# Optimization experiments

Hardware: AMD Instinct MI355X
Metric: run time of the kernel (lower is better)

The kernel has to match this reference:

```python
import jax, jax.numpy as jnp
import numpy as np

NUM_GROUPS = 32
EPS = 1e-5
NUM_HEAD = 8
DIM_HEAD = 64


def group_norm(t, w, b):
    # t: (B, N, C) tokens; GroupNorm over (N, C//G) within each group
    B, N, C = t.shape
    g = t.reshape(B, N, NUM_GROUPS, C // NUM_GROUPS)
    mu = g.mean(axis=(1, 3), keepdims=True)
    var = g.var(axis=(1, 3), keepdims=True)
    g = (g - mu) * jax.lax.rsqrt(var + EPS)
    return g.reshape(B, N, C) * w + b


def setup_inputs() -> dict:
    key = jax.random.key(0)
    ks = jax.random.split(key, 4)
    B, C, H, W = 2, 512, 48, 48
    hidden = NUM_HEAD * DIM_HEAD
    return {
        "x": jax.random.normal(ks[0], (B, C, H, W), dtype=jnp.float32),
        "gn1_w": jnp.ones((C,), jnp.float32),
        "gn1_b": jnp.zeros((C,), jnp.float32),
        "w_qkv": jax.random.normal(ks[1], (3 * hidden, C), jnp.float32) * 0.02,
        "mem_kv": jax.random.normal(ks[2], (2, NUM_HEAD, DIM_HEAD, 4), jnp.float32),
        "w_out": jax.random.normal(ks[3], (C, hidden), jnp.float32) * 0.02,
        "b_out": jnp.zeros((C,), jnp.float32),
        "gn2_w": jnp.ones((C,), jnp.float32),
        "gn2_b": jnp.zeros((C,), jnp.float32),
    }


def reference(x, gn1_w, gn1_b, w_qkv, mem_kv, w_out, b_out, gn2_w, gn2_b):
    B, C, H, W = x.shape
    N = H * W
    hidden = NUM_HEAD * DIM_HEAD
    scale = DIM_HEAD ** -0.5

    # tokens: (B, N, C)
    t = x.reshape(B, C, N).transpose(0, 2, 1)
    t = group_norm(t, gn1_w, gn1_b)

    # 1x1 conv QKV projection == per-token GEMM
    qkv = t @ w_qkv.T  # (B, N, 3*hidden)
    q, k, v = jnp.split(qkv, 3, axis=-1)

    def to_heads(a):  # (B, N, hidden) -> (B, nh, N, dh)
        return a.reshape(B, N, NUM_HEAD, DIM_HEAD).transpose(0, 2, 1, 3)

    q, k, v = to_heads(q), to_heads(k), to_heads(v)

    # memory kv prepended along sequence axis: (nh, dh, nkv) -> (1, nh, nkv, dh)
    mk = jnp.broadcast_to(mem_kv[0].transpose(0, 2, 1)[None], (B, NUM_HEAD, mem_kv.shape[-1], DIM_HEAD))
    mv = jnp.broadcast_to(mem_kv[1].transpose(0, 2, 1)[None], (B, NUM_HEAD, mem_kv.shape[-1], DIM_HEAD))
    k = jnp.concatenate([mk, k], axis=2)
    v = jnp.concatenate([mv, v], axis=2)

    scores = jnp.einsum('bhid,bhjd->bhij', q, k) * scale  # (B, nh, N, N+nkv)
    attn = jax.nn.softmax(scores, axis=-1)  # dropout = identity in eval
    o = jnp.einsum('bhij,bhjd->bhid', attn, v)  # (B, nh, N, dh)

    o = o.transpose(0, 2, 1, 3).reshape(B, N, hidden)
    o = o @ w_out.T + b_out  # 1x1 out conv
    o = group_norm(o, gn2_w, gn2_b)
    return o.transpose(0, 2, 1).reshape(B, C, H, W)
```

## Files before the change

### kernel.cpp

```cpp
#include <hip/hip_runtime.h>
#include <hip/hip_bf16.h>

typedef short short8 __attribute__((ext_vector_type(8)));
typedef float f32x4 __attribute__((ext_vector_type(4)));

#define GPTR(x) ((const __attribute__((address_space(1))) void*)(x))
#define LPTR(x) ((__attribute__((address_space(3))) void*)(x))

static __device__ __forceinline__ unsigned short f2bf(float f) {
  __hip_bfloat16 h = __float2bfloat16(f);
  return __builtin_bit_cast(unsigned short, h);
}
static __device__ __forceinline__ float bf2f(unsigned short u) {
  unsigned int v = ((unsigned int)u) << 16;
  return __builtin_bit_cast(float, v);
}

static __device__ __forceinline__ void block_reduce2(float& s, float& q) {
#pragma unroll
  for (int o = 32; o > 0; o >>= 1) { s += __shfl_down(s, o); q += __shfl_down(q, o); }
  __shared__ float rs[4], rq[4];
  int tid = threadIdx.x;
  if ((tid & 63) == 0) { rs[tid >> 6] = s; rq[tid >> 6] = q; }
  __syncthreads();
  if (tid == 0) {
    s = rs[0] + rs[1] + rs[2] + rs[3];
    q = rq[0] + rq[1] + rq[2] + rq[3];
  }
}

__global__ __launch_bounds__(256) void prep_gn1_kernel(
    const float* __restrict__ wqkv, const float* __restrict__ wout,
    const float* __restrict__ memkv, const float* __restrict__ x,
    unsigned short* __restrict__ wq, unsigned short* __restrict__ wo,
    unsigned short* __restrict__ Kb, unsigned short* __restrict__ Vb,
    float2* __restrict__ part1) {
  int blk = blockIdx.x;
  if (blk < 4128) {
    int i = blk * 256 + threadIdx.x;
    if (i < 786432) {
      wq[i] = f2bf(wqkv[i]);
    } else if (i < 1048576) {
      int j = i - 786432;
      wo[j] = f2bf(wout[j]);
    } else if (i < 1056768) {
      int t = i - 1048576;
      int d = t & 63, j = (t >> 6) & 3, h = (t >> 8) & 7, b = (t >> 11) & 1, s = t >> 12;
      unsigned short bv = f2bf(memkv[((s * 8 + h) * 64 + d) * 4 + j]);
      unsigned short* dst = (s == 0) ? Kb : Vb;
      dst[((size_t)(b * 8 + h) * 2308 + j) * 64 + d] = bv;
    }
  } else {
    int bgc = blk - 4128;
    const float4* base = (const float4*)x + (size_t)bgc * 1152;
    float s = 0.f, q = 0.f;
    for (int i = threadIdx.x; i < 1152; i += 256) {
      float4 v = base[i];
      s += v.x + v.y + v.z + v.w;
      q += v.x * v.x + v.y * v.y + v.z * v.z + v.w * v.w;
    }
    block_reduce2(s, q);
    if (threadIdx.x == 0) part1[bgc] = make_float2(s, q);
  }
}

__global__ __launch_bounds__(256) void tnorm_kernel(const float* __restrict__ x,
    const float* __restrict__ gw, const float* __restrict__ gb,
    const float2* __restrict__ part1, unsigned short* __restrict__ t) {
  __shared__ float tile[32][33];
  int n0 = blockIdx.x * 32, c0 = blockIdx.y * 32, b = blockIdx.z;
  int g0 = c0 >> 4;
  float mu2[2], rs2[2];
#pragma unroll
  for (int gg = 0; gg < 2; gg++) {
    float s = 0.f, q = 0.f;
    const float2* p = part1 + (size_t)(b * 32 + g0 + gg) * 8;
#pragma unroll
    for (int k = 0; k < 8; k++) { float2 v = p[k]; s += v.x; q += v.y; }
    float mu = s / 36864.f;
    float var = q / 36864.f - mu * mu;
    mu2[gg] = mu;
    rs2[gg] = rsqrtf(var + 1e-5f);
  }
  int tx = threadIdx.x & 31, ty = threadIdx.x >> 5;
#pragma unroll
  for (int r = 0; r < 4; r++) {
    int c = c0 + ty + r * 8;
    tile[ty + r * 8][tx] = x[((size_t)(b * 512 + c)) * 2304 + n0 + tx];
  }
  __syncthreads();
  int gg = tx >> 4;
#pragma unroll
  for (int r = 0; r < 4; r++) {
    int n = n0 + ty + r * 8;
    int c = c0 + tx;
    float v = tile[tx][ty + r * 8];
    t[((size_t)(b * 2304 + n)) * 512 + c] = f2bf((v - mu2[gg]) * rs2[gg] * gw[c] + gb[c]);
  }
}

__global__ __launch_bounds__(256) void gemm_qkv_kernel(
    const unsigned short* __restrict__ A, const unsigned short* __restrict__ Bw,
    unsigned short* __restrict__ Qb, unsigned short* __restrict__ Kb,
    unsigned short* __restrict__ Vb) {
  __shared__ __attribute__((aligned(16))) unsigned short As[128 * 32];
  __shared__ __attribute__((aligned(16))) unsigned short Bs[128 * 32];
  int m0 = blockIdx.x * 128, o0 = blockIdx.y * 128;
  int tid = threadIdx.x, lane = tid & 63, wave = tid >> 6;
  int quad = lane >> 4, l15 = lane & 15;
  int wm = wave & 1, wn = wave >> 1;
  f32x4 acc[4][4] = {};
  for (int k0 = 0; k0 < 512; k0 += 32) {
    __syncthreads();
#pragma unroll
    for (int c = 0; c < 2; c++) {
      int q = tid + c * 256;
      int row = q >> 2, cc = q & 3;
      __builtin_amdgcn_global_load_lds(GPTR(A + (size_t)(m0 + row) * 512 + k0 + cc * 8),
                                       LPTR(As + q * 8), 16, 0, 0);
      __builtin_amdgcn_global_load_lds(GPTR(Bw + (size_t)(o0 + row) * 512 + k0 + cc * 8),
                                       LPTR(Bs + q * 8), 16, 0, 0);
    }
    __syncthreads();
    short8 af[4], bf[4];
#pragma unroll
    for (int i = 0; i < 4; i++) af[i] = *(const short8*)(As + (wm * 64 + i * 16 + l15) * 32 + quad * 8);
#pragma unroll
    for (int j = 0; j < 4; j++) bf[j] = *(const short8*)(Bs + (wn * 64 + j * 16 + l15) * 32 + quad * 8);
#pragma unroll
    for (int i = 0; i < 4; i++)
#pragma unroll
      for (int j = 0; j < 4; j++)
        acc[i][j] = __builtin_amdgcn_mfma_f32_16x16x32_bf16(af[i], bf[j], acc[i][j], 0, 0, 0);
  }
#pragma unroll
  for (int i = 0; i < 4; i++) {
#pragma unroll
    for (int j = 0; j < 4; j++) {
      int colo = o0 + wn * 64 + j * 16 + l15;
      int part = colo >> 9, rr = colo & 511, h = rr >> 6, d = rr & 63;
#pragma unroll
      for (int reg = 0; reg < 4; reg++) {
        int m = m0 + wm * 64 + i * 16 + quad * 4 + reg;
        int b = (m >= 2304) ? 1 : 0;
        int n = m - b * 2304;
        unsigned short bv = f2bf(acc[i][j][reg]);
        if (part == 0)      Qb[((size_t)(b * 8 + h) * 2304 + n) * 64 + d] = bv;
        else if (part == 1) Kb[((size_t)(b * 8 + h) * 2308 + 4 + n) * 64 + d] = bv;
        else                Vb[((size_t)(b * 8 + h) * 2308 + 4 + n) * 64 + d] = bv;
      }
    }
  }
}

__global__ __launch_bounds__(256) void vt_kernel(const unsigned short* __restrict__ Vb,
                                                 unsigned short* __restrict__ Vt) {
  __shared__ unsigned short tile[64 * 68];
  int ct = blockIdx.x, bh = blockIdx.y;
  int tid = threadIdx.x;
#pragma unroll
  for (int c = 0; c < 2; c++) {
    int q = tid + c * 256;
    int row = q >> 3, c8 = q & 7;
    int gk = ct * 64 + row;
    uint4 v = make_uint4(0, 0, 0, 0);
    if (gk < 2308) v = *(const uint4*)(Vb + ((size_t)bh * 2308 + gk) * 64 + c8 * 8);
    *(uint2*)(tile + row * 68 + c8 * 8)     = make_uint2(v.x, v.y);
    *(uint2*)(tile + row * 68 + c8 * 8 + 4) = make_uint2(v.z, v.w);
  }
  __syncthreads();
#pragma unroll
  for (int c = 0; c < 2; c++) {
    int q = tid + c * 256;
    int d = q >> 3, c8 = q & 7;
    unsigned short tmp[8];
#pragma unroll
    for (int jj = 0; jj < 8; jj++) tmp[jj] = tile[(c8 * 8 + jj) * 68 + d];
    *(uint4*)(Vt + ((size_t)bh * 64 + d) * 2368 + ct * 64 + c8 * 8) = *(uint4*)tmp;
  }
}

__global__ __launch_bounds__(256) void attn_kernel(
    const unsigned short* __restrict__ Qb, const unsigned short* __restrict__ Kb,
    const unsigned short* __restrict__ Vt,
    unsigned short* __restrict__ Opart, float* __restrict__ Lbuf) {
  __shared__ __attribute__((aligned(16))) unsigned short Ks[64 * 72];
  __shared__ __attribute__((aligned(16))) unsigned short Vts[64 * 72];
  __shared__ __attribute__((aligned(16))) unsigned short Ps[128 * 72];
  int qt = blockIdx.x, bh = blockIdx.y, sp = blockIdx.z;
  int m0 = qt * 128;
  int kt0 = sp * 10, kt1 = (kt0 + 10 < 37) ? kt0 + 10 : 37;
  const unsigned short* Qh = Qb + (size_t)bh * 2304 * 64;
  const unsigned short* Kh = Kb + (size_t)bh * 2308 * 64;
  const unsigned short* VtH = Vt + (size_t)bh * 64 * 2368;
  int tid = threadIdx.x, lane = tid & 63, wave = tid >> 6;
  int quad = lane >> 4, l15 = lane & 15;
  const float CS = 0.18033688011112042f;

  short8 qf[2][2];
#pragma unroll
  for (int i = 0; i < 2; i++)
#pragma unroll
    for (int s = 0; s < 2; s++)
      qf[i][s] = *(const short8*)(Qh + (size_t)(m0 + wave * 32 + i * 16 + l15) * 64 + s * 32 + quad * 8);

  f32x4 oacc[2][4] = {};
  float lsum[2][4] = {};

  for (int kt = kt0; kt < kt1; kt++) {
    __syncthreads();
#pragma unroll
    for (int c = 0; c < 2; c++) {
      int q = tid + c * 256;
      int krow = q >> 3, c8 = q & 7;
      int gk = kt * 64 + krow;
      uint4 kv = make_uint4(0, 0, 0, 0);
      if (gk < 2308) kv = *(const uint4*)(Kh + (size_t)gk * 64 + c8 * 8);
      *(uint4*)(Ks + krow * 72 + c8 * 8) = kv;
      uint4 vv = *(const uint4*)(VtH + (size_t)krow * 2368 + kt * 64 + c8 * 8);
      *(uint4*)(Vts + krow * 72 + c8 * 8) = vv;
    }
    __syncthreads();
    f32x4 sacc[2][4] = {};
#pragma unroll
    for (int s = 0; s < 2; s++) {
      short8 kf[4];
#pragma unroll
      for (int j = 0; j < 4; j++) kf[j] = *(const short8*)(Ks + (j * 16 + l15) * 72 + s * 32 + quad * 8);
#pragma unroll
      for (int i = 0; i < 2; i++)
#pragma unroll
        for (int j = 0; j < 4; j++)
          sacc[i][j] = __builtin_amdgcn_mfma_f32_16x16x32_bf16(qf[i][s], kf[j], sacc[i][j], 0, 0, 0);
    }
    if (kt == 36) {
#pragma unroll
      for (int j = 0; j < 4; j++) {
        bool ok = (kt * 64 + j * 16 + l15) < 2308;
        if (!ok) {
#pragma unroll
          for (int i = 0; i < 2; i++)
#pragma unroll
            for (int r = 0; r < 4; r++) sacc[i][j][r] = -1e30f;
        }
      }
    }
#pragma unroll
    for (int i = 0; i < 2; i++) {
#pragma unroll
      for (int r = 0; r < 4; r++) {
        int prow = (wave * 32 + i * 16 + quad * 4 + r) * 72;
#pragma unroll
        for (int j = 0; j < 4; j++) {
          float p = exp2f(sacc[i][j][r] * CS);
          lsum[i][r] += p;
          Ps[prow + j * 16 + l15] = f2bf(p);
        }
      }
    }
#pragma unroll
    for (int s = 0; s < 2; s++) {
      short8 ap[2];
#pragma unroll
      for (int i = 0; i < 2; i++)
        ap[i] = *(const short8*)(Ps + (wave * 32 + i * 16 + l15) * 72 + s * 32 + quad * 8);
#pragma unroll
      for (int jo = 0; jo < 4; jo++) {
        short8 bv = *(const short8*)(Vts + (jo * 16 + l15) * 72 + s * 32 + quad * 8);
#pragma unroll
        for (int i = 0; i < 2; i++)
          oacc[i][jo] = __builtin_amdgcn_mfma_f32_16x16x32_bf16(ap[i], bv, oacc[i][jo], 0, 0, 0);
      }
    }
  }
#pragma unroll
  for (int i = 0; i < 2; i++)
#pragma unroll
    for (int r = 0; r < 4; r++) {
      float v = lsum[i][r];
#pragma unroll
      for (int o = 1; o < 16; o <<= 1) v += __shfl_xor(v, o);
      lsum[i][r] = v;
    }
  size_t obase = (size_t)(sp * 16 + bh) * 2304;
#pragma unroll
  for (int i = 0; i < 2; i++) {
#pragma unroll
    for (int r = 0; r < 4; r++) {
      int row = m0 + wave * 32 + i * 16 + quad * 4 + r;
#pragma unroll
      for (int jo = 0; jo < 4; jo++)
        Opart[(obase + row) * 64 + jo * 16 + l15] = f2bf(oacc[i][jo][r]);
      if (l15 == 0) Lbuf[obase + row] = lsum[i][r];
    }
  }
}

__global__ __launch_bounds__(256) void combine_kernel(
    const unsigned short* __restrict__ Opart, const float* __restrict__ Lbuf,
    unsigned short* __restrict__ Ot) {
  int rg = blockIdx.x * 4 + (threadIdx.x >> 6);
  int d = threadIdx.x & 63;
  int bh = rg / 2304, row = rg - bh * 2304;
  int b = bh >> 3, h = bh & 7;
  float num = 0.f, den = 0.f;
#pragma unroll
  for (int s = 0; s < 4; s++) {
    size_t ri = ((size_t)(s * 16 + bh) * 2304 + row);
    den += Lbuf[ri];
    num += bf2f(Opart[ri * 64 + d]);
  }
  Ot[((size_t)(b * 2304 + row)) * 512 + h * 64 + d] = f2bf(num / den);
}

__global__ __launch_bounds__(256) void gemm_out_kernel(
    const unsigned short* __restrict__ A, const unsigned short* __restrict__ Bw,
    const float* __restrict__ bias, float* __restrict__ y,
    float* __restrict__ p2s, float* __restrict__ p2q) {
  __shared__ __attribute__((aligned(16))) unsigned short As[128 * 32];
  __shared__ __attribute__((aligned(16))) unsigned short Bs[128 * 32];
  __shared__ float sgrp[8], qgrp[8];
  int m0 = blockIdx.x * 128, o0 = blockIdx.y * 128;
  int tid = threadIdx.x, lane = tid & 63, wave = tid >> 6;
  int quad = lane >> 4, l15 = lane & 15;
  int wm = wave & 1, wn = wave >> 1;
  if (tid < 8) { sgrp[tid] = 0.f; qgrp[tid] = 0.f; }
  f32x4 acc[4][4] = {};
  for (int k0 = 0; k0 < 512; k0 += 32) {
    __syncthreads();
#pragma unroll
    for (int c = 0; c < 2; c++) {
      int q = tid + c * 256;
      int row = q >> 2, cc = q & 3;
      __builtin_amdgcn_global_load_lds(GPTR(A + (size_t)(m0 + row) * 512 + k0 + cc * 8),
                                       LPTR(As + q * 8), 16, 0, 0);
      __builtin_amdgcn_global_load_lds(GPTR(Bw + (size_t)(o0 + row) * 512 + k0 + cc * 8),
                                       LPTR(Bs + q * 8), 16, 0, 0);
    }
    __syncthreads();
    short8 af[4], bf[4];
#pragma unroll
    for (int i = 0; i < 4; i++) af[i] = *(const short8*)(As + (wm * 64 + i * 16 + l15) * 32 + quad * 8);
#pragma unroll
    for (int j = 0; j < 4; j++) bf[j] = *(const short8*)(Bs + (wn * 64 + j * 16 + l15) * 32 + quad * 8);
#pragma unroll
    for (int i = 0; i < 4; i++)
#pragma unroll
      for (int j = 0; j < 4; j++)
        acc[i][j] = __builtin_amdgcn_mfma_f32_16x16x32_bf16(af[i], bf[j], acc[i][j], 0, 0, 0);
  }
  float ss[4] = {}, qq[4] = {};
#pragma unroll
  for (int i = 0; i < 4; i++) {
#pragma unroll
    for (int j = 0; j < 4; j++) {
      int colo = o0 + wn * 64 + j * 16 + l15;
      float bb = bias[colo];
#pragma unroll
      for (int reg = 0; reg < 4; reg++) {
        int m = m0 + wm * 64 + i * 16 + quad * 4 + reg;
        float v = acc[i][j][reg] + bb;
        y[(size_t)m * 512 + colo] = v;
        ss[j] += v;
        qq[j] += v * v;
      }
    }
  }
#pragma unroll
  for (int j = 0; j < 4; j++) {
#pragma unroll
    for (int o = 1; o < 64; o <<= 1) { ss[j] += __shfl_xor(ss[j], o); qq[j] += __shfl_xor(qq[j], o); }
  }
  if (lane == 0) {
#pragma unroll
    for (int j = 0; j < 4; j++) {
      atomicAdd(&sgrp[wn * 4 + j], ss[j]);
      atomicAdd(&qgrp[wn * 4 + j], qq[j]);
    }
  }
  __syncthreads();
  if (tid < 8) {
    int b = (m0 >= 2304) ? 1 : 0;
    int g = b * 32 + (o0 >> 4) + tid;
    atomicAdd(&p2s[g], sgrp[tid]);
    atomicAdd(&p2q[g], qgrp[tid]);
  }
}

__global__ __launch_bounds__(256) void gn2_final_kernel(const float* __restrict__ y,
    const float* __restrict__ gw, const float* __restrict__ gb,
    const float* __restrict__ p2s, const float* __restrict__ p2q,
    float* __restrict__ out) {
  __shared__ float tile[32][33];
  int n0 = blockIdx.x * 32, c0 = blockIdx.y * 32, b = blockIdx.z;
  int g0 = c0 >> 4;
  float mu2[2], rs2[2];
#pragma unroll
  for (int gg = 0; gg < 2; gg++) {
    float s = p2s[b * 32 + g0 + gg], q = p2q[b * 32 + g0 + gg];
    float mu = s / 36864.f;
    float var = q / 36864.f - mu * mu;
    mu2[gg] = mu;
    rs2[gg] = rsqrtf(var + 1e-5f);
  }
  int tx = threadIdx.x & 31, ty = threadIdx.x >> 5;
#pragma unroll
  for (int r = 0; r < 4; r++) {
    int n = n0 + ty + r * 8;
    tile[ty + r * 8][tx] = y[((size_t)(b * 2304 + n)) * 512 + c0 + tx];
  }
  __syncthreads();
#pragma unroll
  for (int r = 0; r < 4; r++) {
    int c = c0 + ty + r * 8;
    int gg = (ty + r * 8) >> 4;
    float v = tile[tx][ty + r * 8];
    out[((size_t)(b * 512 + c)) * 2304 + n0 + tx] = (v - mu2[gg]) * rs2[gg] * gw[c] + gb[c];
  }
}

extern "C" void kernel_launch(void* const* d_in, const int* in_sizes, int n_in,
                              void* d_out, int out_size, void* d_ws, size_t ws_size,
                              hipStream_t stream) {
  const float* x     = (const float*)d_in[0];
  const float* gn1w  = (const float*)d_in[1];
  const float* gn1b  = (const float*)d_in[2];
  const float* wqkv  = (const float*)d_in[3];
  const float* memkv = (const float*)d_in[4];
  const float* wout  = (const float*)d_in[5];
  const float* bout  = (const float*)d_in[6];
  const float* gn2w  = (const float*)d_in[7];
  const float* gn2b  = (const float*)d_in[8];
  float* out = (float*)d_out;

  char* ws = (char*)d_ws;
  float2* part1        = (float2*)(ws + 0);
  float* p2s           = (float*)(ws + 4096);
  float* p2q           = (float*)(ws + 4352);
  unsigned short* wqB  = (unsigned short*)(ws + 69632);
  unsigned short* woB  = (unsigned short*)(ws + 1642496);
  unsigned short* tB   = (unsigned short*)(ws + 2166784);
  unsigned short* Qb   = (unsigned short*)(ws + 6885376);
  unsigned short* Kb   = (unsigned short*)(ws + 11603968);
  unsigned short* Vb   = (unsigned short*)(ws + 16330752);
  unsigned short* Ot   = (unsigned short*)(ws + 21057536);
  float* y             = (float*)(ws + 25776128);
  unsigned short* Vt   = (unsigned short*)(ws + 35213312);
  unsigned short* Opart= (unsigned short*)(ws + 40062976);
  float* Lbuf          = (float*)(ws + 58937344);

  prep_gn1_kernel<<<4640, 256, 0, stream>>>(wqkv, wout, memkv, x, wqB, woB, Kb, Vb, part1);
  tnorm_kernel<<<dim3(72, 16, 2), 256, 0, stream>>>(x, gn1w, gn1b, part1, tB);
  gemm_qkv_kernel<<<dim3(36, 12), 256, 0, stream>>>(tB, wqB, Qb, Kb, Vb);
  vt_kernel<<<dim3(37, 16), 256, 0, stream>>>(Vb, Vt);
  attn_kernel<<<dim3(18, 16, 4), 256, 0, stream>>>(Qb, Kb, Vt, Opart, Lbuf);
  combine_kernel<<<9216, 256, 0, stream>>>(Opart, Lbuf, Ot);
  hipMemsetAsync(ws + 4096, 0, 512, stream);
  gemm_out_kernel<<<dim3(36, 4), 256, 0, stream>>>(Ot, woB, bout, y, p2s, p2q);
  gn2_final_kernel<<<dim3(72, 16, 2), 256, 0, stream>>>(y, gn2w, gn2b, p2s, p2q, out);
}
```

Measured before the change: 193.8 us.

## Write V transposed from QKV GEMM, fuse prep into tnorm, vectorize combine

The QKV GEMM epilogue now writes V straight into the transposed Vt layout, and the separate vt transpose kernel and the Vb buffer are removed. The weight conversion and memory-kv setup are merged into the tnorm kernel launch, and the GN1 statistics move to their own small kernel. The combine kernel now handles four channels per thread with vector loads and stores. Together these cut one launch and one round trip of V through memory. The risk is that the Vt padding columns past the real key length are no longer zeroed explicitly, and the GEMM epilogue's transposed stores are strided.

```diff
diff --git a/kernel.cpp b/kernel.cpp
--- a/kernel.cpp
+++ b/kernel.cpp
@@ -29,80 +29,80 @@
   }
 }
 
-__global__ __launch_bounds__(256) void prep_gn1_kernel(
+__global__ __launch_bounds__(256) void gn1_stats_kernel(const float* __restrict__ x,
+                                                        float2* __restrict__ part1) {
+  int bgc = blockIdx.x;
+  const float4* base = (const float4*)x + (size_t)bgc * 1152;
+  float s = 0.f, q = 0.f;
+  for (int i = threadIdx.x; i < 1152; i += 256) {
+    float4 v = base[i];
+    s += v.x + v.y + v.z + v.w;
+    q += v.x * v.x + v.y * v.y + v.z * v.z + v.w * v.w;
+  }
+  block_reduce2(s, q);
+  if (threadIdx.x == 0) part1[bgc] = make_float2(s, q);
+}
+
+__global__ __launch_bounds__(256) void tnorm_prep_kernel(const float* __restrict__ x,
+    const float* __restrict__ gw, const float* __restrict__ gb,
+    const float2* __restrict__ part1, unsigned short* __restrict__ t,
     const float* __restrict__ wqkv, const float* __restrict__ wout,
-    const float* __restrict__ memkv, const float* __restrict__ x,
+    const float* __restrict__ memkv,
     unsigned short* __restrict__ wq, unsigned short* __restrict__ wo,
-    unsigned short* __restrict__ Kb, unsigned short* __restrict__ Vb,
-    float2* __restrict__ part1) {
+    unsigned short* __restrict__ Kb, unsigned short* __restrict__ Vt) {
+  __shared__ float tile[32][33];
   int blk = blockIdx.x;
-  if (blk < 4128) {
-    int i = blk * 256 + threadIdx.x;
+  if (blk < 2304) {
+    int n0 = (blk % 72) * 32, c0 = ((blk / 72) & 15) * 32, b = blk / 1152;
+    int g0 = c0 >> 4;
+    float mu2[2], rs2[2];
+#pragma unroll
+    for (int gg = 0; gg < 2; gg++) {
+      float s = 0.f, q = 0.f;
+      const float2* p = part1 + (size_t)(b * 32 + g0 + gg) * 8;
+#pragma unroll
+      for (int k = 0; k < 8; k++) { float2 v = p[k]; s += v.x; q += v.y; }
+      float mu = s / 36864.f;
+      float var = q / 36864.f - mu * mu;
+      mu2[gg] = mu;
+      rs2[gg] = rsqrtf(var + 1e-5f);
+    }
+    int tx = threadIdx.x & 31, ty = threadIdx.x >> 5;
+#pragma unroll
+    for (int r = 0; r < 4; r++) {
+      int c = c0 + ty + r * 8;
+      tile[ty + r * 8][tx] = x[((size_t)(b * 512 + c)) * 2304 + n0 + tx];
+    }
+    __syncthreads();
+    int gg = tx >> 4;
+#pragma unroll
+    for (int r = 0; r < 4; r++) {
+      int n = n0 + ty + r * 8;
+      int c = c0 + tx;
+      float v = tile[tx][ty + r * 8];
+      t[((size_t)(b * 2304 + n)) * 512 + c] = f2bf((v - mu2[gg]) * rs2[gg] * gw[c] + gb[c]);
+    }
+  } else {
+    int i = (blk - 2304) * 256 + threadIdx.x;
     if (i < 786432) {
       wq[i] = f2bf(wqkv[i]);
     } else if (i < 1048576) {
       int j = i - 786432;
       wo[j] = f2bf(wout[j]);
     } else if (i < 1056768) {
-      int t = i - 1048576;
-      int d = t & 63, j = (t >> 6) & 3, h = (t >> 8) & 7, b = (t >> 11) & 1, s = t >> 12;
+      int tt = i - 1048576;
+      int d = tt & 63, j = (tt >> 6) & 3, h = (tt >> 8) & 7, b = (tt >> 11) & 1, s = tt >> 12;
       unsigned short bv = f2bf(memkv[((s * 8 + h) * 64 + d) * 4 + j]);
-      unsigned short* dst = (s == 0) ? Kb : Vb;
-      dst[((size_t)(b * 8 + h) * 2308 + j) * 64 + d] = bv;
-    }
-  } else {
-    int bgc = blk - 4128;
-    const float4* base = (const float4*)x + (size_t)bgc * 1152;
-    float s = 0.f, q = 0.f;
-    for (int i = threadIdx.x; i < 1152; i += 256) {
-      float4 v = base[i];
-      s += v.x + v.y + v.z + v.w;
-      q += v.x * v.x + v.y * v.y + v.z * v.z + v.w * v.w;
-    }
-    block_reduce2(s, q);
-    if (threadIdx.x == 0) part1[bgc] = make_float2(s, q);
-  }
-}
-
-__global__ __launch_bounds__(256) void tnorm_kernel(const float* __restrict__ x,
-    const float* __restrict__ gw, const float* __restrict__ gb,
-    const float2* __restrict__ part1, unsigned short* __restrict__ t) {
-  __shared__ float tile[32][33];
-  int n0 = blockIdx.x * 32, c0 = blockIdx.y * 32, b = blockIdx.z;
-  int g0 = c0 >> 4;
-  float mu2[2], rs2[2];
-#pragma unroll
-  for (int gg = 0; gg < 2; gg++) {
-    float s = 0.f, q = 0.f;
-    const float2* p = part1 + (size_t)(b * 32 + g0 + gg) * 8;
-#pragma unroll
-    for (int k = 0; k < 8; k++) { float2 v = p[k]; s += v.x; q += v.y; }
-    float mu = s / 36864.f;
-    float var = q / 36864.f - mu * mu;
-    mu2[gg] = mu;
-    rs2[gg] = rsqrtf(var + 1e-5f);
-  }
-  int tx = threadIdx.x & 31, ty = threadIdx.x >> 5;
-#pragma unroll
-  for (int r = 0; r < 4; r++) {
-    int c = c0 + ty + r * 8;
-    tile[ty + r * 8][tx] = x[((size_t)(b * 512 + c)) * 2304 + n0 + tx];
-  }
-  __syncthreads();
-  int gg = tx >> 4;
-#pragma unroll
-  for (int r = 0; r < 4; r++) {
-    int n = n0 + ty + r * 8;
-    int c = c0 + tx;
-    float v = tile[tx][ty + r * 8];
-    t[((size_t)(b * 2304 + n)) * 512 + c] = f2bf((v - mu2[gg]) * rs2[gg] * gw[c] + gb[c]);
+      if (s == 0) Kb[((size_t)(b * 8 + h) * 2308 + j) * 64 + d] = bv;
+      else        Vt[((size_t)(b * 8 + h) * 64 + d) * 2368 + j] = bv;
+    }
   }
 }
 
 __global__ __launch_bounds__(256) void gemm_qkv_kernel(
     const unsigned short* __restrict__ A, const unsigned short* __restrict__ Bw,
     unsigned short* __restrict__ Qb, unsigned short* __restrict__ Kb,
-    unsigned short* __restrict__ Vb) {
+    unsigned short* __restrict__ Vt) {
   __shared__ __attribute__((aligned(16))) unsigned short As[128 * 32];
   __shared__ __attribute__((aligned(16))) unsigned short Bs[128 * 32];
   int m0 = blockIdx.x * 128, o0 = blockIdx.y * 128;
@@ -139,44 +139,26 @@
     for (int j = 0; j < 4; j++) {
       int colo = o0 + wn * 64 + j * 16 + l15;
       int part = colo >> 9, rr = colo & 511, h = rr >> 6, d = rr & 63;
-#pragma unroll
-      for (int reg = 0; reg < 4; reg++) {
-        int m = m0 + wm * 64 + i * 16 + quad * 4 + reg;
-        int b = (m >= 2304) ? 1 : 0;
-        int n = m - b * 2304;
-        unsigned short bv = f2bf(acc[i][j][reg]);
-        if (part == 0)      Qb[((size_t)(b * 8 + h) * 2304 + n) * 64 + d] = bv;
-        else if (part == 1) Kb[((size_t)(b * 8 + h) * 2308 + 4 + n) * 64 + d] = bv;
-        else                Vb[((size_t)(b * 8 + h) * 2308 + 4 + n) * 64 + d] = bv;
+      int mbase = m0 + wm * 64 + i * 16 + quad * 4;
+      int b = (mbase >= 2304) ? 1 : 0;
+      int n = mbase - b * 2304;
+      unsigned short bv[4];
+#pragma unroll
+      for (int reg = 0; reg < 4; reg++) bv[reg] = f2bf(acc[i][j][reg]);
+      if (part == 0) {
+#pragma unroll
+        for (int reg = 0; reg < 4; reg++)
+          Qb[((size_t)(b * 8 + h) * 2304 + n + reg) * 64 + d] = bv[reg];
+      } else if (part == 1) {
+#pragma unroll
+        for (int reg = 0; reg < 4; reg++)
+          Kb[((size_t)(b * 8 + h) * 2308 + 4 + n + reg) * 64 + d] = bv[reg];
+      } else {
+        unsigned long long pk = (unsigned long long)bv[0] | ((unsigned long long)bv[1] << 16) |
+                                ((unsigned long long)bv[2] << 32) | ((unsigned long long)bv[3] << 48);
+        *(unsigned long long*)(Vt + ((size_t)(b * 8 + h) * 64 + d) * 2368 + 4 + n) = pk;
       }
     }
-  }
-}
-
-__global__ __launch_bounds__(256) void vt_kernel(const unsigned short* __restrict__ Vb,
-                                                 unsigned short* __restrict__ Vt) {
-  __shared__ unsigned short tile[64 * 68];
-  int ct = blockIdx.x, bh = blockIdx.y;
-  int tid = threadIdx.x;
-#pragma unroll
-  for (int c = 0; c < 2; c++) {
-    int q = tid + c * 256;
-    int row = q >> 3, c8 = q & 7;
-    int gk = ct * 64 + row;
-    uint4 v = make_uint4(0, 0, 0, 0);
-    if (gk < 2308) v = *(const uint4*)(Vb + ((size_t)bh * 2308 + gk) * 64 + c8 * 8);
-    *(uint2*)(tile + row * 68 + c8 * 8)     = make_uint2(v.x, v.y);
-    *(uint2*)(tile + row * 68 + c8 * 8 + 4) = make_uint2(v.z, v.w);
-  }
-  __syncthreads();
-#pragma unroll
-  for (int c = 0; c < 2; c++) {
-    int q = tid + c * 256;
-    int d = q >> 3, c8 = q & 7;
-    unsigned short tmp[8];
-#pragma unroll
-    for (int jj = 0; jj < 8; jj++) tmp[jj] = tile[(c8 * 8 + jj) * 68 + d];
-    *(uint4*)(Vt + ((size_t)bh * 64 + d) * 2368 + ct * 64 + c8 * 8) = *(uint4*)tmp;
   }
 }
 
@@ -299,18 +281,26 @@
 __global__ __launch_bounds__(256) void combine_kernel(
     const unsigned short* __restrict__ Opart, const float* __restrict__ Lbuf,
     unsigned short* __restrict__ Ot) {
-  int rg = blockIdx.x * 4 + (threadIdx.x >> 6);
-  int d = threadIdx.x & 63;
+  int t = threadIdx.x;
+  int rg = blockIdx.x * 16 + (t >> 4);
+  int d4 = (t & 15) * 4;
   int bh = rg / 2304, row = rg - bh * 2304;
   int b = bh >> 3, h = bh & 7;
-  float num = 0.f, den = 0.f;
+  float den = 0.f, num[4] = {};
 #pragma unroll
   for (int s = 0; s < 4; s++) {
     size_t ri = ((size_t)(s * 16 + bh) * 2304 + row);
     den += Lbuf[ri];
-    num += bf2f(Opart[ri * 64 + d]);
-  }
-  Ot[((size_t)(b * 2304 + row)) * 512 + h * 64 + d] = f2bf(num / den);
+    uint2 pv = *(const uint2*)(Opart + ri * 64 + d4);
+    const unsigned short* pp = (const unsigned short*)&pv;
+#pragma unroll
+    for (int k = 0; k < 4; k++) num[k] += bf2f(pp[k]);
+  }
+  float rinv = 1.f / den;
+  unsigned short ov[4];
+#pragma unroll
+  for (int k = 0; k < 4; k++) ov[k] = f2bf(num[k] * rinv);
+  *(uint2*)(Ot + ((size_t)(b * 2304 + row)) * 512 + h * 64 + d4) = *(uint2*)ov;
 }
 
 __global__ __launch_bounds__(256) void gemm_out_kernel(
@@ -442,19 +432,18 @@
   unsigned short* tB   = (unsigned short*)(ws + 2166784);
   unsigned short* Qb   = (unsigned short*)(ws + 6885376);
   unsigned short* Kb   = (unsigned short*)(ws + 11603968);
-  unsigned short* Vb   = (unsigned short*)(ws + 16330752);
   unsigned short* Ot   = (unsigned short*)(ws + 21057536);
   float* y             = (float*)(ws + 25776128);
   unsigned short* Vt   = (unsigned short*)(ws + 35213312);
   unsigned short* Opart= (unsigned short*)(ws + 40062976);
   float* Lbuf          = (float*)(ws + 58937344);
 
-  prep_gn1_kernel<<<4640, 256, 0, stream>>>(wqkv, wout, memkv, x, wqB, woB, Kb, Vb, part1);
-  tnorm_kernel<<<dim3(72, 16, 2), 256, 0, stream>>>(x, gn1w, gn1b, part1, tB);
-  gemm_qkv_kernel<<<dim3(36, 12), 256, 0, stream>>>(tB, wqB, Qb, Kb, Vb);
-  vt_kernel<<<dim3(37, 16), 256, 0, stream>>>(Vb, Vt);
+  gn1_stats_kernel<<<512, 256, 0, stream>>>(x, part1);
+  tnorm_prep_kernel<<<6432, 256, 0, stream>>>(x, gn1w, gn1b, part1, tB,
+                                              wqkv, wout, memkv, wqB, woB, Kb, Vt);
+  gemm_qkv_kernel<<<dim3(36, 12), 256, 0, stream>>>(tB, wqB, Qb, Kb, Vt);
   attn_kernel<<<dim3(18, 16, 4), 256, 0, stream>>>(Qb, Kb, Vt, Opart, Lbuf);
-  combine_kernel<<<9216, 256, 0, stream>>>(Opart, Lbuf, Ot);
+  combine_kernel<<<2304, 256, 0, stream>>>(Opart, Lbuf, Ot);
   hipMemsetAsync(ws + 4096, 0, 512, stream);
   gemm_out_kernel<<<dim3(36, 4), 256, 0, stream>>>(Ot, woB, bout, y, p2s, p2q);
   gn2_final_kernel<<<dim3(72, 16, 2), 256, 0, stream>>>(y, gn2w, gn2b, p2s, p2q, out);
```

Result: faster. 182.2 us (-5.9%).
